# Kernel optimization log

Measured on AMD Instinct MI355X. Metric: run time of the kernel, lower is better.

Reference implementation:

```python
import jax, jax.numpy as jnp
import numpy as np

N_NODES = 100000
N_EDGES = 1600000
D_IN = 128
NEG_SLOPE = 0.2


def setup_inputs() -> dict:
    key = jax.random.key(0)
    ks = jax.random.split(key, 12)
    x = jax.random.normal(ks[0], (N_NODES, D_IN), dtype=jnp.float32)
    edge_index = jax.random.randint(ks[1], (2, N_EDGES), 0, N_NODES, dtype=jnp.int64)
    s = 0.1
    # layer 1: in=128, out=16, heads=2
    W1 = jax.random.normal(ks[2], (D_IN, 2 * 16), dtype=jnp.float32) * s
    att_src1 = jax.random.normal(ks[3], (2, 16), dtype=jnp.float32) * s
    att_dst1 = jax.random.normal(ks[4], (2, 16), dtype=jnp.float32) * s
    b1 = jnp.zeros((32,), dtype=jnp.float32)
    # layer 2: in=32, out=2, heads=1
    W2 = jax.random.normal(ks[5], (32, 1 * 2), dtype=jnp.float32) * s
    att_src2 = jax.random.normal(ks[6], (1, 2), dtype=jnp.float32) * s
    att_dst2 = jax.random.normal(ks[7], (1, 2), dtype=jnp.float32) * s
    b2 = jnp.zeros((2,), dtype=jnp.float32)
    return {"x": x, "edge_index": edge_index, "W1": W1, "att_src1": att_src1,
            "att_dst1": att_dst1, "b1": b1, "W2": W2, "att_src2": att_src2,
            "att_dst2": att_dst2, "b2": b2}


def gat_conv(x, src, dst, W, a_src, a_dst, b, heads, out_dim):
    n = x.shape[0]
    h = (x @ W).reshape(n, heads, out_dim)            # [N,H,F]
    alpha_src = jnp.sum(h * a_src, axis=-1)            # [N,H]
    alpha_dst = jnp.sum(h * a_dst, axis=-1)            # [N,H]
    e = jax.nn.leaky_relu(alpha_src[src] + alpha_dst[dst], NEG_SLOPE)  # [E,H]
    # segment softmax over destination neighborhoods
    m = jax.ops.segment_max(e, dst, num_segments=n)
    e = jnp.exp(e - m[dst])
    denom = jax.ops.segment_sum(e, dst, num_segments=n)
    alpha = e / (denom[dst] + 1e-16)                   # [E,H]
    msg = h[src] * alpha[:, :, None]                   # [E,H,F]
    out = jax.ops.segment_sum(msg, dst, num_segments=n)
    return out.reshape(n, heads * out_dim) + b


def reference(x, edge_index, W1, att_src1, att_dst1, b1, W2, att_src2, att_dst2, b2):
    n = x.shape[0]
    loops = jnp.arange(n, dtype=edge_index.dtype)
    ei = jnp.concatenate([edge_index, jnp.stack([loops, loops])], axis=1)
    src, dst = ei[0], ei[1]
    h = gat_conv(x, src, dst, W1, att_src1, att_dst1, b1, heads=2, out_dim=16)
    h = jax.nn.relu(h)
    out = gat_conv(h, src, dst, W2, att_src2, att_dst2, b2, heads=1, out_dim=2)
    return out
```

## Files before the change

kernel.cpp:

```cpp
#include <hip/hip_runtime.h>
#include <hip/hip_fp16.h>
#include <float.h>

#define NN 100000
#define NE 1600000
#define NB 391
#define NBLK 512
#define CHUNK 3125
#define TOT (NB * NBLK)
#define SCAN_B2 ((TOT + 255) / 256)
#define NODE1_B 1563
#define MAXB 12288
#define XPAD 136

typedef _Float16 f16x8 __attribute__((ext_vector_type(8)));
typedef _Float16 f16x4 __attribute__((ext_vector_type(4)));
typedef float f32x4 __attribute__((ext_vector_type(4)));


__device__ __forceinline__ void load_edge(const int* __restrict__ ei, int is64,
                                          int idx, int& s, int& d) {
    if (is64) {
        const long long* e64 = (const long long*)ei;
        s = (int)e64[idx]; d = (int)e64[NE + idx];
    } else {
        s = ei[idx]; d = ei[NE + idx];
    }
}

__device__ __forceinline__ int load_dst(const int* __restrict__ ei, int is64, int idx) {
    if (is64) return (int)((const long long*)ei)[NE + idx];
    return ei[NE + idx];
}

__device__ __forceinline__ int detect64(const int* __restrict__ ei, int t, int* s_flag) {
    if (t < 64) {
        unsigned w = ((const unsigned*)ei)[t];
        unsigned long long m = __ballot((t & 1) && w != 0);
        if (t == 0) *s_flag = (m == 0) ? 1 : 0;
    }
    __syncthreads();
    return *s_flag;
}

__device__ __forceinline__ f16x8 load_bfrag(const float* __restrict__ W1,
                                            int n, int c, int g, int col) {
    f16x8 b;
    #pragma unroll
    for (int i = 0; i < 8; ++i)
        b[i] = (_Float16)W1[(c * 32 + g * 8 + i) * 32 + n * 16 + col];
    return b;
}


__global__ __launch_bounds__(256) void k_hist_node1(
    const int* __restrict__ ei, int* __restrict__ hist_g,
    const float* __restrict__ x, const float* __restrict__ W1,
    const float* __restrict__ att_d,
    uint4* __restrict__ h1r, float* __restrict__ ad1) {
    __shared__ __align__(16) char arena[64 * XPAD * 2];
    __shared__ int s_flag;
    int t = threadIdx.x;
    if (blockIdx.x < NBLK) {
        int* h = (int*)arena;
        for (int i = t; i < NB; i += 256) h[i] = 0;
        int is64 = detect64(ei, t, &s_flag);
        int base = blockIdx.x * CHUNK;
        for (int k = t; k < CHUNK; k += 256) {
            int d = load_dst(ei, is64, base + k);
            atomicAdd(&h[d >> 8], 1);
        }
        __syncthreads();
        for (int i = t; i < NB; i += 256) hist_g[i * NBLK + blockIdx.x] = h[i];
    } else {
        _Float16* xs = (_Float16*)arena;
        int row0 = (blockIdx.x - NBLK) * 64;
        const float4* xg = (const float4*)x;
        #pragma unroll
        for (int i = 0; i < 8; ++i) {
            int f = i * 256 + t;
            int row = f >> 5, c4 = f & 31;
            int gr = row0 + row; if (gr >= NN) gr = NN - 1;
            float4 v = xg[(size_t)gr * 32 + c4];
            f16x4 hv = {(_Float16)v.x, (_Float16)v.y, (_Float16)v.z, (_Float16)v.w};
            *(f16x4*)(xs + row * XPAD + c4 * 4) = hv;
        }
        int w = t >> 6, lane = t & 63;
        int g = lane >> 4, col = lane & 15;
        const f16x8 b00 = load_bfrag(W1, 0, 0, g, col);
        const f16x8 b01 = load_bfrag(W1, 0, 1, g, col);
        const f16x8 b02 = load_bfrag(W1, 0, 2, g, col);
        const f16x8 b03 = load_bfrag(W1, 0, 3, g, col);
        const f16x8 b10 = load_bfrag(W1, 1, 0, g, col);
        const f16x8 b11 = load_bfrag(W1, 1, 1, g, col);
        const f16x8 b12 = load_bfrag(W1, 1, 2, g, col);
        const f16x8 b13 = load_bfrag(W1, 1, 3, g, col);
        float at0 = att_d[col];
        float at1 = att_d[16 + col];
        __syncthreads();
        const _Float16* xrow = xs + (w * 16 + col) * XPAD;
        f16x8 a0 = *(const f16x8*)(xrow + 0 * 32 + g * 8);
        f16x8 a1 = *(const f16x8*)(xrow + 1 * 32 + g * 8);
        f16x8 a2 = *(const f16x8*)(xrow + 2 * 32 + g * 8);
        f16x8 a3 = *(const f16x8*)(xrow + 3 * 32 + g * 8);
        f32x4 acc0 = {0.f, 0.f, 0.f, 0.f};
        f32x4 acc1 = {0.f, 0.f, 0.f, 0.f};
        acc0 = __builtin_amdgcn_mfma_f32_16x16x32_f16(a0, b00, acc0, 0, 0, 0);
        acc0 = __builtin_amdgcn_mfma_f32_16x16x32_f16(a1, b01, acc0, 0, 0, 0);
        acc0 = __builtin_amdgcn_mfma_f32_16x16x32_f16(a2, b02, acc0, 0, 0, 0);
        acc0 = __builtin_amdgcn_mfma_f32_16x16x32_f16(a3, b03, acc0, 0, 0, 0);
        acc1 = __builtin_amdgcn_mfma_f32_16x16x32_f16(a0, b10, acc1, 0, 0, 0);
        acc1 = __builtin_amdgcn_mfma_f32_16x16x32_f16(a1, b11, acc1, 0, 0, 0);
        acc1 = __builtin_amdgcn_mfma_f32_16x16x32_f16(a2, b12, acc1, 0, 0, 0);
        acc1 = __builtin_amdgcn_mfma_f32_16x16x32_f16(a3, b13, acc1, 0, 0, 0);
        _Float16* h1h = (_Float16*)h1r;
        int rbase = row0 + w * 16;
        #pragma unroll
        for (int reg = 0; reg < 4; ++reg) {
            float v0 = acc0[reg], v1 = acc1[reg];
            int grow = rbase + g * 4 + reg;
            bool ok = grow < NN;
            if (ok) {
                h1h[grow * 32 + col]      = (_Float16)v0;
                h1h[grow * 32 + 16 + col] = (_Float16)v1;
            }
            float p0 = v0 * at0, p1 = v1 * at1;
            #pragma unroll
            for (int off = 1; off <= 8; off <<= 1) {
                p0 += __shfl_xor(p0, off);
                p1 += __shfl_xor(p1, off);
            }
            if (ok && col == 0) {
                ad1[grow * 2]     = p0;
                ad1[grow * 2 + 1] = p1;
            }
        }
    }
}


__global__ __launch_bounds__(256) void k_scan1(const int* __restrict__ hist_g,
                                               int* __restrict__ bsum) {
    __shared__ int part[4];
    int t = threadIdx.x;
    int i = blockIdx.x * 256 + t;
    int v = (i < TOT) ? hist_g[i] : 0;
    #pragma unroll
    for (int off = 32; off; off >>= 1) v += __shfl_xor(v, off);
    if ((t & 63) == 0) part[t >> 6] = v;
    __syncthreads();
    if (t == 0) bsum[blockIdx.x] = part[0] + part[1] + part[2] + part[3];
}


__global__ __launch_bounds__(256) void k_scan3(const int* __restrict__ hist_g,
                                               const int* __restrict__ bsum,
                                               int* __restrict__ hist_s,
                                               int* __restrict__ bbase) {
    __shared__ int red[4];
    __shared__ int s[256];
    int t = threadIdx.x, b = blockIdx.x;
    int partial = 0;
    for (int i = t; i < b; i += 256) partial += bsum[i];
    #pragma unroll
    for (int off = 32; off; off >>= 1) partial += __shfl_xor(partial, off);
    if ((t & 63) == 0) red[t >> 6] = partial;
    int i = b * 256 + t;
    int v = (i < TOT) ? hist_g[i] : 0;
    s[t] = v;
    __syncthreads();
    int boff = red[0] + red[1] + red[2] + red[3];
    for (int off = 1; off < 256; off <<= 1) {
        int u = (t >= off) ? s[t - off] : 0;
        __syncthreads();
        s[t] += u;
        __syncthreads();
    }
    if (i < TOT) {
        int e = boff + s[t] - v;
        hist_s[i] = e;
        if ((i & (NBLK - 1)) == 0) bbase[i / NBLK] = e;
    }
    if (b == 0 && t == 0) bbase[NB] = NE;
}


__global__ __launch_bounds__(512) void k_part(const int* __restrict__ ei,
                                              const int* __restrict__ hist_s,
                                              unsigned* __restrict__ pairs) {
    __shared__ int cur[NB];
    __shared__ int s_flag;
    int t = threadIdx.x;
    for (int i = t; i < NB; i += 512) cur[i] = hist_s[i * NBLK + blockIdx.x];
    int is64 = detect64(ei, t, &s_flag);
    int base = blockIdx.x * CHUNK;
    for (int k = t; k < CHUNK; k += 512) {
        int s, d; load_edge(ei, is64, base + k, s, d);
        int p = atomicAdd(&cur[d >> 8], 1);
        pairs[p] = ((unsigned)s << 8) | (unsigned)(d & 255);
    }
}


__global__ __launch_bounds__(256) void k_csr(const unsigned* __restrict__ pairs,
                                             const int* __restrict__ bbase,
                                             int* __restrict__ offs,
                                             int* __restrict__ srcs) {
    __shared__ unsigned plds[MAXB];
    __shared__ int cnt_l[256];
    __shared__ int scan_l[256];
    int b = blockIdx.x, t = threadIdx.x;
    int beg = bbase[b], end = bbase[b + 1];
    int m = end - beg;
    if (m > MAXB) m = MAXB;
    for (int k = t; k < m; k += 256) plds[k] = pairs[beg + k];
    cnt_l[t] = 0;
    __syncthreads();
    for (int k = t; k < m; k += 256) atomicAdd(&cnt_l[plds[k] & 255], 1);
    __syncthreads();
    int v = cnt_l[t];
    scan_l[t] = v;
    __syncthreads();
    for (int off = 1; off < 256; off <<= 1) {
        int u = (t >= off) ? scan_l[t - off] : 0;
        __syncthreads();
        scan_l[t] += u;
        __syncthreads();
    }
    int lexcl = scan_l[t] - v;
    int node = (b << 8) + t;
    if (node < NN) offs[node] = beg + lexcl;
    if (b == 0 && t == 0) offs[NN] = NE;
    cnt_l[t] = lexcl;
    __syncthreads();
    for (int k = t; k < m; k += 256) {
        unsigned e = plds[k];
        int p = atomicAdd(&cnt_l[e & 255], 1);
        srcs[beg + p] = (int)(e >> 8);
    }
}


__global__ __launch_bounds__(256) void k_agg1(
    const int* __restrict__ offs, const int* __restrict__ srcs,
    const float2* __restrict__ ad1, const uint2* __restrict__ h1x,
    const float* __restrict__ att_s, const float* __restrict__ b1,
    const float* __restrict__ W2, const float* __restrict__ as2w,
    const float* __restrict__ ad2w, uint2* __restrict__ hx) {
    int n = (blockIdx.x * blockDim.x + threadIdx.x) >> 4;
    if (n >= NN) return;
    int lane = threadIdx.x & 63;
    int r = lane & 15;
    int eg = r >> 3;
    int j4 = r & 7;
    float4 av = ((const float4*)att_s)[j4];
    int beg = offs[n];
    int deg = offs[n + 1] - beg;
    int tot = deg + 1;
    float2 adp = ad1[n];
    float adh = (j4 < 4) ? adp.x : adp.y;
    float ac0 = 0.f, ac1 = 0.f, ac2 = 0.f, ac3 = 0.f, dsum = 0.f;
    int k = eg;
    int s0 = (k < tot) ? ((k < deg) ? srcs[beg + k] : n) : 0;
    uint2 v0 = h1x[s0 * 8 + j4];
    for (; k < tot; k += 2) {
        int kn = k + 2;
        int s1 = (kn < tot) ? ((kn < deg) ? srcs[beg + kn] : n) : 0;
        uint2 v1 = h1x[s1 * 8 + j4];
        float2 fa = __half22float2(*(__half2*)&v0.x);
        float2 fb = __half22float2(*(__half2*)&v0.y);
        float tsum = fa.x * av.x + fa.y * av.y + fb.x * av.z + fb.y * av.w;
        tsum += __shfl_xor(tsum, 1);
        tsum += __shfl_xor(tsum, 2);
        float e = tsum + adh;
        e = fmaxf(e, 0.2f * e);
        float p = __expf(e);
        ac0 = fmaf(p, fa.x, ac0);
        ac1 = fmaf(p, fa.y, ac1);
        ac2 = fmaf(p, fb.x, ac2);
        ac3 = fmaf(p, fb.y, ac3);
        if ((j4 & 3) == 0) dsum += p;
        s0 = s1; v0 = v1;
    }
    ac0 += __shfl_xor(ac0, 8);
    ac1 += __shfl_xor(ac1, 8);
    ac2 += __shfl_xor(ac2, 8);
    ac3 += __shfl_xor(ac3, 8);
    dsum += __shfl_xor(dsum, 8);
    float denom = __shfl(dsum, (lane & 0x30) | (j4 & 4));
    float inv = 1.f / (denom + 1e-16f);
    float4 bb = ((const float4*)b1)[j4];
    float r0 = fmaxf(ac0 * inv + bb.x, 0.f);
    float r1 = fmaxf(ac1 * inv + bb.y, 0.f);
    float r2 = fmaxf(ac2 * inv + bb.z, 0.f);
    float r3 = fmaxf(ac3 * inv + bb.w, 0.f);
    float4 wA = ((const float4*)W2)[2 * j4];
    float4 wB = ((const float4*)W2)[2 * j4 + 1];
    float c0 = r0 * wA.x + r1 * wA.z + r2 * wB.x + r3 * wB.z;
    float c1 = r0 * wA.y + r1 * wA.w + r2 * wB.y + r3 * wB.w;
    #pragma unroll
    for (int off = 4; off; off >>= 1) {
        c0 += __shfl_xor(c0, off);
        c1 += __shfl_xor(c1, off);
    }
    if (r == 0) {
        float a_s = c0 * as2w[0] + c1 * as2w[1];
        float a_d = c0 * ad2w[0] + c1 * ad2w[1];
        __half2 lo = __floats2half2_rn(c0, c1);
        __half2 hi = __floats2half2_rn(a_s, a_d);
        uint2 pk;
        pk.x = *(unsigned*)&lo;
        pk.y = *(unsigned*)&hi;
        hx[n] = pk;
    }
}


__global__ __launch_bounds__(256) void k_agg2(
    const int* __restrict__ offs, const int* __restrict__ srcs,
    const uint2* __restrict__ hx, const float* __restrict__ b2,
    float* __restrict__ out) {
    int n = (blockIdx.x * blockDim.x + threadIdx.x) >> 4;
    if (n >= NN) return;
    int lane = threadIdx.x & 15;
    int beg = offs[n];
    int deg = offs[n + 1] - beg;
    uint2 mynode = hx[n];
    __half2 myhi = *(__half2*)&mynode.y;
    float adv = __high2float(myhi);
    float dsum = 0.f, s0acc = 0.f, s1acc = 0.f;
    int k = lane;
    int s0 = (k <= deg) ? ((k < deg) ? srcs[beg + k] : n) : 0;
    uint2 r0 = hx[s0];
    for (; k <= deg; k += 16) {
        int kn = k + 16;
        int s1 = (kn <= deg) ? ((kn < deg) ? srcs[beg + kn] : n) : 0;
        uint2 r1 = hx[s1];
        __half2 lo = *(__half2*)&r0.x;
        __half2 hi = *(__half2*)&r0.y;
        float e = __low2float(hi) + adv;
        e = fmaxf(e, 0.2f * e);
        float p = __expf(e);
        dsum += p;
        s0acc = fmaf(p, __low2float(lo), s0acc);
        s1acc = fmaf(p, __high2float(lo), s1acc);
        r0 = r1;
    }
    #pragma unroll
    for (int off = 8; off; off >>= 1) {
        dsum  += __shfl_xor(dsum, off, 16);
        s0acc += __shfl_xor(s0acc, off, 16);
        s1acc += __shfl_xor(s1acc, off, 16);
    }
    if (lane == 0) {
        float inv = 1.f / (dsum + 1e-16f);
        out[n * 2]     = s0acc * inv + b2[0];
        out[n * 2 + 1] = s1acc * inv + b2[1];
    }
}


extern "C" void kernel_launch(void* const* d_in, const int* in_sizes, int n_in,
                              void* d_out, int out_size, void* d_ws, size_t ws_size,
                              hipStream_t stream) {
    const float* x    = (const float*)d_in[0];
    const int*   ei   = (const int*)d_in[1];
    const float* W1   = (const float*)d_in[2];
    const float* as1w = (const float*)d_in[3];
    const float* ad1w = (const float*)d_in[4];
    const float* b1   = (const float*)d_in[5];
    const float* W2   = (const float*)d_in[6];
    const float* as2w = (const float*)d_in[7];
    const float* ad2w = (const float*)d_in[8];
    const float* b2   = (const float*)d_in[9];
    float* out = (float*)d_out;

    float* ws = (float*)d_ws;
    uint4* h1r = (uint4*)ws; ws += 16 * NN;
    float* ad1 = ws; ws += 2 * NN;
    uint2* hx  = (uint2*)ws; ws += 2 * NN;
    int* offs   = (int*)ws; ws += NN + 1;
    int* srcs   = (int*)ws; ws += NE;
    int* hist_g = (int*)ws; ws += TOT;
    int* hist_s = (int*)ws; ws += TOT;
    int* bsum   = (int*)ws; ws += SCAN_B2;
    int* bbase  = (int*)ws; ws += NB + 1;
    unsigned* pairs = (unsigned*)srcs;

    k_hist_node1<<<NBLK + NODE1_B, 256, 0, stream>>>(ei, hist_g, x, W1, ad1w, h1r, ad1);
    k_scan1<<<SCAN_B2, 256, 0, stream>>>(hist_g, bsum);
    k_scan3<<<SCAN_B2, 256, 0, stream>>>(hist_g, bsum, hist_s, bbase);
    k_part<<<NBLK, 512, 0, stream>>>(ei, hist_s, pairs);
    k_csr<<<NB, 256, 0, stream>>>(pairs, bbase, offs, srcs);
    k_agg1<<<6250, 256, 0, stream>>>(offs, srcs, (const float2*)ad1, (const uint2*)h1r,
                                     as1w, b1, W2, as2w, ad2w, hx);
    k_agg2<<<6250, 256, 0, stream>>>(offs, srcs, hx, b2, out);
}
```

Baseline: 93.66 us.

## Store self-loops in CSR and narrow layer-2 aggregation to 8 lanes per node

The CSR build now writes each node's self-loop as an explicit entry at the end of its neighbour list, so offsets span NE+NN entries. This removes the per-edge branches that synthesized the self-loop in both aggregation kernels, which now use clamped index loads. The pairs buffer gets its own workspace region instead of aliasing srcs, since the two no longer fit in the same space. Layer-2 aggregation uses 8 lanes per node instead of 16, halving the grid, to cut idle lanes at an average degree of about 17.

```diff
diff --git a/kernel.cpp b/kernel.cpp
--- a/kernel.cpp
+++ b/kernel.cpp
@@ -227,16 +227,19 @@
         scan_l[t] += u;
         __syncthreads();
     }
-    int lexcl = scan_l[t] - v;
     int node = (b << 8) + t;
-    if (node < NN) offs[node] = beg + lexcl;
-    if (b == 0 && t == 0) offs[NN] = NE;
-    cnt_l[t] = lexcl;
+    int pos = beg + (b << 8) + (scan_l[t] - v) + t;
+    if (node < NN) {
+        offs[node] = pos;
+        srcs[pos + v] = node;
+    }
+    if (b == 0 && t == 0) offs[NN] = NE + NN;
+    cnt_l[t] = pos;
     __syncthreads();
     for (int k = t; k < m; k += 256) {
         unsigned e = plds[k];
         int p = atomicAdd(&cnt_l[e & 255], 1);
-        srcs[beg + p] = (int)(e >> 8);
+        srcs[p] = (int)(e >> 8);
     }
 }
 
@@ -255,17 +258,16 @@
     int j4 = r & 7;
     float4 av = ((const float4*)att_s)[j4];
     int beg = offs[n];
-    int deg = offs[n + 1] - beg;
-    int tot = deg + 1;
+    int end = offs[n + 1];
+    int last = end - 1;
     float2 adp = ad1[n];
     float adh = (j4 < 4) ? adp.x : adp.y;
     float ac0 = 0.f, ac1 = 0.f, ac2 = 0.f, ac3 = 0.f, dsum = 0.f;
-    int k = eg;
-    int s0 = (k < tot) ? ((k < deg) ? srcs[beg + k] : n) : 0;
+    int k = beg + eg;
+    int s0 = srcs[min(k, last)];
     uint2 v0 = h1x[s0 * 8 + j4];
-    for (; k < tot; k += 2) {
-        int kn = k + 2;
-        int s1 = (kn < tot) ? ((kn < deg) ? srcs[beg + kn] : n) : 0;
+    for (; k < end; k += 2) {
+        int s1 = srcs[min(k + 2, last)];
         uint2 v1 = h1x[s1 * 8 + j4];
         float2 fa = __half22float2(*(__half2*)&v0.x);
         float2 fb = __half22float2(*(__half2*)&v0.y);
@@ -320,21 +322,21 @@
     const int* __restrict__ offs, const int* __restrict__ srcs,
     const uint2* __restrict__ hx, const float* __restrict__ b2,
     float* __restrict__ out) {
-    int n = (blockIdx.x * blockDim.x + threadIdx.x) >> 4;
+    int n = (blockIdx.x * blockDim.x + threadIdx.x) >> 3;
     if (n >= NN) return;
-    int lane = threadIdx.x & 15;
+    int r = threadIdx.x & 7;
     int beg = offs[n];
-    int deg = offs[n + 1] - beg;
+    int end = offs[n + 1];
+    int last = end - 1;
     uint2 mynode = hx[n];
     __half2 myhi = *(__half2*)&mynode.y;
     float adv = __high2float(myhi);
     float dsum = 0.f, s0acc = 0.f, s1acc = 0.f;
-    int k = lane;
-    int s0 = (k <= deg) ? ((k < deg) ? srcs[beg + k] : n) : 0;
+    int k = beg + r;
+    int s0 = srcs[min(k, last)];
     uint2 r0 = hx[s0];
-    for (; k <= deg; k += 16) {
-        int kn = k + 16;
-        int s1 = (kn <= deg) ? ((kn < deg) ? srcs[beg + kn] : n) : 0;
+    for (; k < end; k += 8) {
+        int s1 = srcs[min(k + 8, last)];
         uint2 r1 = hx[s1];
         __half2 lo = *(__half2*)&r0.x;
         __half2 hi = *(__half2*)&r0.y;
@@ -347,12 +349,12 @@
         r0 = r1;
     }
     #pragma unroll
-    for (int off = 8; off; off >>= 1) {
-        dsum  += __shfl_xor(dsum, off, 16);
-        s0acc += __shfl_xor(s0acc, off, 16);
-        s1acc += __shfl_xor(s1acc, off, 16);
-    }
-    if (lane == 0) {
+    for (int off = 4; off; off >>= 1) {
+        dsum  += __shfl_xor(dsum, off);
+        s0acc += __shfl_xor(s0acc, off);
+        s1acc += __shfl_xor(s1acc, off);
+    }
+    if (r == 0) {
         float inv = 1.f / (dsum + 1e-16f);
         out[n * 2]     = s0acc * inv + b2[0];
         out[n * 2 + 1] = s1acc * inv + b2[1];
@@ -380,12 +382,12 @@
     float* ad1 = ws; ws += 2 * NN;
     uint2* hx  = (uint2*)ws; ws += 2 * NN;
     int* offs   = (int*)ws; ws += NN + 1;
-    int* srcs   = (int*)ws; ws += NE;
+    int* srcs   = (int*)ws; ws += NE + NN + 16;
+    unsigned* pairs = (unsigned*)ws; ws += NE;
     int* hist_g = (int*)ws; ws += TOT;
     int* hist_s = (int*)ws; ws += TOT;
     int* bsum   = (int*)ws; ws += SCAN_B2;
     int* bbase  = (int*)ws; ws += NB + 1;
-    unsigned* pairs = (unsigned*)srcs;
 
     k_hist_node1<<<NBLK + NODE1_B, 256, 0, stream>>>(ei, hist_g, x, W1, ad1w, h1r, ad1);
     k_scan1<<<SCAN_B2, 256, 0, stream>>>(hist_g, bsum);
@@ -394,5 +396,5 @@
     k_csr<<<NB, 256, 0, stream>>>(pairs, bbase, offs, srcs);
     k_agg1<<<6250, 256, 0, stream>>>(offs, srcs, (const float2*)ad1, (const uint2*)h1r,
                                      as1w, b1, W2, as2w, ad2w, hx);
-    k_agg2<<<6250, 256, 0, stream>>>(offs, srcs, hx, b2, out);
-}
+    k_agg2<<<3125, 256, 0, stream>>>(offs, srcs, hx, b2, out);
+}
```

Result: slower. 105.4 us, median of 2 (+12.5%).
